# Performance work log

Hardware: AMD Instinct MI355X
Metric: run time of the kernel (lower is better)

## Reference

```python
import jax, jax.numpy as jnp
import numpy as np

B, SQ, SK, D, H, HD = 2, 2048, 2048, 1024, 16, 64


def setup_inputs() -> dict:
    key = jax.random.key(0)
    ks = jax.random.split(key, 10)
    s = 1.0 / np.sqrt(D)  # keep activations well-scaled
    return {
        "x": jax.random.normal(ks[0], (B, SQ, D), jnp.float32),
        "encoder_output": jax.random.normal(ks[1], (B, SK, D), jnp.float32),
        "Wq": jax.random.normal(ks[2], (H, D, HD), jnp.float32) * s,
        "bq": jax.random.normal(ks[3], (H, HD), jnp.float32) * 0.01,
        "Wk": jax.random.normal(ks[4], (H, D, HD), jnp.float32) * s,
        "bk": jax.random.normal(ks[5], (H, HD), jnp.float32) * 0.01,
        "Wv": jax.random.normal(ks[6], (H, D, HD), jnp.float32) * s,
        "bv": jax.random.normal(ks[7], (H, HD), jnp.float32) * 0.01,
        "Wo": jax.random.normal(ks[8], (D, D), jnp.float32) * s,
        "bo": jax.random.normal(ks[9], (D,), jnp.float32) * 0.01,
    }


def reference(x, encoder_output, Wq, bq, Wk, bk, Wv, bv, Wo, bo):
    # Batched per-head projections (equivalent to the per-head nn.Linear loop).
    q = jnp.einsum('bsd,hde->bhse', x, Wq) + bq[None, :, None, :]              # [B,H,SQ,HD]
    k = jnp.einsum('bsd,hde->bhse', encoder_output, Wk) + bk[None, :, None, :]  # [B,H,SK,HD]
    v = jnp.einsum('bsd,hde->bhse', encoder_output, Wv) + bv[None, :, None, :]  # [B,H,SK,HD]
    scale = 1.0 / jnp.sqrt(jnp.asarray(HD, q.dtype))
    scores = jnp.einsum('bhqe,bhke->bhqk', q, k) * scale                        # [B,H,SQ,SK]
    attn = jax.nn.softmax(scores, axis=-1)
    out = jnp.einsum('bhqk,bhke->bhqe', attn, v)                                # [B,H,SQ,HD]
    # concat heads along feature dim (head order matches torch.cat order)
    out = out.transpose(0, 2, 1, 3).reshape(out.shape[0], out.shape[2], -1)     # [B,SQ,D]
    # final linear; dropout is identity in eval mode
    return out @ Wo + bo
```

## Files before the change

### kernel.cpp

```cpp
#include <hip/hip_runtime.h>


typedef unsigned short u16;
typedef __bf16 bf16x8 __attribute__((ext_vector_type(8)));
typedef float f32x4 __attribute__((ext_vector_type(4)));
typedef float f32x16 __attribute__((ext_vector_type(16)));
typedef unsigned u32x2 __attribute__((ext_vector_type(2)));

#define B_ 2
#define SQ_ 2048
#define SK_ 2048
#define D_ 1024
#define H_ 16
#define HD_ 64

__device__ __forceinline__ u16 f2bf(float f) {
  union { float f; unsigned u; } c; c.f = f;
  unsigned u = c.u;
  return (u16)((u + 0x7fffu + ((u >> 16) & 1u)) >> 16);
}
__device__ __forceinline__ float bf2f(u16 h) {
  union { unsigned u; float f; } c; c.u = ((unsigned)h) << 16;
  return c.f;
}
__device__ __forceinline__ unsigned pack_bf16(float lo, float hi) {
  union { __bf16 h[2]; unsigned u; } c;
  c.h[0] = (__bf16)lo;
  c.h[1] = (__bf16)hi;
  return c.u;
}

#define GLOAD_LDS16(gp, lp)                                                  \
  __builtin_amdgcn_global_load_lds(                                          \
      (const __attribute__((address_space(1))) void*)(gp),                   \
      (__attribute__((address_space(3))) void*)(lp), 16, 0, 0)

__global__ __launch_bounds__(256) void prep_fused(const float* __restrict__ x,
                                                  const float* __restrict__ enc,
                                                  const float* __restrict__ Wq,
                                                  const float* __restrict__ Wk,
                                                  const float* __restrict__ Wv,
                                                  const float* __restrict__ Wo,
                                                  u16* __restrict__ xb,
                                                  u16* __restrict__ eb,
                                                  u16* __restrict__ WqT,
                                                  u16* __restrict__ WoT) {
  __shared__ float tile[64][65];
  const int id = blockIdx.x;
  const int tid = threadIdx.x;

  if (id < 8192) {
    const float* in = (id >= 4096) ? enc : x;
    u16* out = (id >= 4096) ? eb : xb;
    int i = (id & 4095) * 256 + tid;
    float4 v = ((const float4*)in)[i];
    uint2 p;
    p.x = (unsigned)f2bf(v.x) | ((unsigned)f2bf(v.y) << 16);
    p.y = (unsigned)f2bf(v.z) | ((unsigned)f2bf(v.w) << 16);
    ((uint2*)out)[i] = p;
    return;
  }

  if (id < 8960) {
    const int f = id - 8192;
    const int z48 = f >> 4, y = f & 15;
    const int mat = z48 >> 4, head = z48 & 15;
    const float* W = (mat == 0) ? Wq : (mat == 1 ? Wk : Wv);
    const float* ib = W + (long)head * 65536;
    u16* ob = WqT + ((long)mat << 20) + (long)head * 65536;
    const int r0 = y << 6;
#pragma unroll
    for (int i = 0; i < 16; ++i) {
      int idx = tid + (i << 8);
      int r = idx >> 6, c = idx & 63;
      tile[r][c] = ib[(long)(r0 + r) * 64 + c];
    }
    __syncthreads();
#pragma unroll
    for (int i = 0; i < 16; ++i) {
      int idx = tid + (i << 8);
      int cc = idx >> 6, rr = idx & 63;
      ob[(long)cc * 1024 + (r0 + rr)] = f2bf(tile[rr][cc]);
    }
    return;
  }

  {
    const int g = id - 8960;
    const int c0 = (g & 15) << 6, r0 = (g >> 4) << 6;
#pragma unroll
    for (int i = 0; i < 16; ++i) {
      int idx = tid + (i << 8);
      int r = idx >> 6, c = idx & 63;
      tile[r][c] = Wo[(long)(r0 + r) * 1024 + (c0 + c)];
    }
    __syncthreads();
#pragma unroll
    for (int i = 0; i < 16; ++i) {
      int idx = tid + (i << 8);
      int cc = idx >> 6, rr = idx & 63;
      WoT[(long)(c0 + cc) * 1024 + (r0 + rr)] = f2bf(tile[rr][cc]);
    }
  }
}

__global__ __launch_bounds__(256) void gemm_qkv(const u16* __restrict__ xb,
                                                const u16* __restrict__ eb,
                                                const u16* __restrict__ Wt3,
                                                const float* __restrict__ bq,
                                                const float* __restrict__ bk,
                                                const float* __restrict__ bv,
                                                u16* __restrict__ qws,
                                                u16* __restrict__ kws,
                                                u16* __restrict__ vT) {
  constexpr int M = 2048, N = 1024, K = 1024;
  __shared__ __align__(16) u16 As[128 * 64];
  __shared__ __align__(16) u16 Bs[128 * 64];
  const int tid = threadIdx.x;
  const int lane = tid & 63;
  const int wid = tid >> 6;
  const int l16 = lane & 15, quad = lane >> 4;
  const int wm = wid >> 1, wn = wid & 1;
  const int bn0g = blockIdx.x << 7;
  const int seg = bn0g >> 10;
  const int bn0 = bn0g & (N - 1);
  const int bm0 = blockIdx.y << 7;
  const u16* A = (seg == 0) ? xb : eb;
  const u16* Wt = Wt3 + ((long)seg << 20);
  const float* bias = (seg == 0) ? bq : (seg == 1 ? bk : bv);
  const long abase = (long)blockIdx.z * M * K;

  f32x4 acc[4][4];
#pragma unroll
  for (int i = 0; i < 4; ++i)
#pragma unroll
    for (int j = 0; j < 4; ++j) acc[i][j] = f32x4{0.f, 0.f, 0.f, 0.f};

  const int r0 = tid >> 3;
  const int c0s = ((tid & 7) ^ (r0 & 7)) << 3;
  const u16* agp = A + abase + (long)(bm0 + r0) * K + c0s;
  const u16* bgp = Wt + (long)(bn0 + r0) * K + c0s;
  u16* alp = As + tid * 8;
  u16* blp = Bs + tid * 8;

  for (int k0 = 0; k0 < K; k0 += 64) {
#pragma unroll
    for (int i = 0; i < 4; ++i) {
      GLOAD_LDS16(agp + k0 + (long)(32 * i) * K, alp + i * 2048);
      GLOAD_LDS16(bgp + k0 + (long)(32 * i) * K, blp + i * 2048);
    }
    __syncthreads();
#pragma unroll
    for (int kk = 0; kk < 2; ++kk) {
      const int csw = ((quad + 4 * kk) ^ (l16 & 7)) << 3;
      bf16x8 af[4], bfr[4];
#pragma unroll
      for (int mi = 0; mi < 4; ++mi)
        af[mi] = *(const bf16x8*)(As + (wm * 64 + mi * 16 + l16) * 64 + csw);
#pragma unroll
      for (int ni = 0; ni < 4; ++ni)
        bfr[ni] = *(const bf16x8*)(Bs + (wn * 64 + ni * 16 + l16) * 64 + csw);
#pragma unroll
      for (int mi = 0; mi < 4; ++mi)
#pragma unroll
        for (int ni = 0; ni < 4; ++ni)
          acc[mi][ni] = __builtin_amdgcn_mfma_f32_16x16x32_bf16(af[mi], bfr[ni],
                                                                acc[mi][ni], 0, 0, 0);
    }
    __syncthreads();
  }

  float bv4[4];
#pragma unroll
  for (int ni = 0; ni < 4; ++ni) bv4[ni] = bias[bn0 + wn * 64 + ni * 16 + l16];

  if (seg == 2) {
    const long zb = (long)blockIdx.z * N * M;
#pragma unroll
    for (int mi = 0; mi < 4; ++mi)
#pragma unroll
      for (int ni = 0; ni < 4; ++ni) {
        int colg = bn0 + wn * 64 + ni * 16 + l16;
        int rowg = bm0 + wm * 64 + mi * 16 + (quad << 2);
        ushort4 pk = make_ushort4(f2bf(acc[mi][ni][0] + bv4[ni]),
                                  f2bf(acc[mi][ni][1] + bv4[ni]),
                                  f2bf(acc[mi][ni][2] + bv4[ni]),
                                  f2bf(acc[mi][ni][3] + bv4[ni]));
        *(ushort4*)(vT + zb + (long)colg * M + rowg) = pk;
      }
  } else {
    u16* outp = seg ? kws : qws;
    const long cbase = (long)blockIdx.z * M * N;
#pragma unroll
    for (int mi = 0; mi < 4; ++mi)
#pragma unroll
      for (int ni = 0; ni < 4; ++ni)
#pragma unroll
        for (int r = 0; r < 4; ++r) {
          int row = bm0 + wm * 64 + mi * 16 + (quad << 2) + r;
          int col = bn0 + wn * 64 + ni * 16 + l16;
          outp[cbase + (long)row * N + col] = f2bf(acc[mi][ni][r] + bv4[ni]);
        }
  }
}

__global__ __launch_bounds__(256) void gemm_final(const u16* __restrict__ A,
                                                  const u16* __restrict__ Wt,
                                                  const float* __restrict__ bias,
                                                  float* __restrict__ C) {
  constexpr int M = 2048, N = 1024, K = 1024;
  __shared__ __align__(16) u16 As[64 * 64];
  __shared__ __align__(16) u16 Bs[128 * 64];
  const int tid = threadIdx.x;
  const int lane = tid & 63;
  const int wid = tid >> 6;
  const int l16 = lane & 15, quad = lane >> 4;
  const int bn0 = blockIdx.x << 7, bm0 = blockIdx.y << 6;

  f32x4 acc[4][2];
#pragma unroll
  for (int i = 0; i < 4; ++i)
#pragma unroll
    for (int j = 0; j < 2; ++j) acc[i][j] = f32x4{0.f, 0.f, 0.f, 0.f};

  const int r0 = tid >> 3;
  const int c0s = ((tid & 7) ^ (r0 & 7)) << 3;
  const long abase = (long)blockIdx.z * M * K;
  const u16* agp = A + abase + (long)(bm0 + r0) * K + c0s;
  const u16* bgp = Wt + (long)(bn0 + r0) * K + c0s;
  u16* alp = As + tid * 8;
  u16* blp = Bs + tid * 8;

  for (int k0 = 0; k0 < K; k0 += 64) {
#pragma unroll
    for (int i = 0; i < 2; ++i)
      GLOAD_LDS16(agp + k0 + (long)(32 * i) * K, alp + i * 2048);
#pragma unroll
    for (int i = 0; i < 4; ++i)
      GLOAD_LDS16(bgp + k0 + (long)(32 * i) * K, blp + i * 2048);
    __syncthreads();
#pragma unroll
    for (int kk = 0; kk < 2; ++kk) {
      const int csw = ((quad + 4 * kk) ^ (l16 & 7)) << 3;
      bf16x8 af[4], bfr[2];
#pragma unroll
      for (int mi = 0; mi < 4; ++mi)
        af[mi] = *(const bf16x8*)(As + (mi * 16 + l16) * 64 + csw);
#pragma unroll
      for (int ni = 0; ni < 2; ++ni)
        bfr[ni] = *(const bf16x8*)(Bs + (wid * 32 + ni * 16 + l16) * 64 + csw);
#pragma unroll
      for (int mi = 0; mi < 4; ++mi)
#pragma unroll
        for (int ni = 0; ni < 2; ++ni)
          acc[mi][ni] = __builtin_amdgcn_mfma_f32_16x16x32_bf16(af[mi], bfr[ni],
                                                                acc[mi][ni], 0, 0, 0);
    }
    __syncthreads();
  }

  float bv2[2];
#pragma unroll
  for (int ni = 0; ni < 2; ++ni) bv2[ni] = bias[bn0 + wid * 32 + ni * 16 + l16];
  const long cbase = (long)blockIdx.z * M * N;
#pragma unroll
  for (int mi = 0; mi < 4; ++mi)
#pragma unroll
    for (int ni = 0; ni < 2; ++ni)
#pragma unroll
      for (int r = 0; r < 4; ++r) {
        int row = bm0 + mi * 16 + (quad << 2) + r;
        int col = bn0 + wid * 32 + ni * 16 + l16;
        C[cbase + (long)row * N + col] = acc[mi][ni][r] + bv2[ni];
      }
}

#define ATTN_STAGE(kbase, vbase)                                              \
  do {                                                                        \
    GLOAD_LDS16(kp, (kbase) + tid * 8);                                       \
    GLOAD_LDS16(kp + (long)32 * D_, (kbase) + 2048 + tid * 8);                \
    GLOAD_LDS16(vp, (vbase) + tid * 8);                                       \
    GLOAD_LDS16(vp + (long)32 * SK_, (vbase) + 2048 + tid * 8);               \
    kp += (long)64 * D_;                                                      \
    vp += 64;                                                                 \
  } while (0)

#define QK_BLOCK(Kb, sx0, sx1)                                                \
  do {                                                                        \
    {                                                                         \
      bf16x8 kf0 = *(const bf16x8*)((Kb) + ro0 + sw[0]);                      \
      bf16x8 kf1 = *(const bf16x8*)((Kb) + 2048 + ro0 + sw[0]);               \
      sx0 = __builtin_amdgcn_mfma_f32_32x32x16_bf16(kf0, qf[0], ZV, 0, 0, 0); \
      sx1 = __builtin_amdgcn_mfma_f32_32x32x16_bf16(kf1, qf[0], ZV, 0, 0, 0); \
    }                                                                         \
    _Pragma("unroll") for (int j = 1; j < 4; ++j) {                           \
      bf16x8 kf0 = *(const bf16x8*)((Kb) + ro0 + sw[j]);                      \
      bf16x8 kf1 = *(const bf16x8*)((Kb) + 2048 + ro0 + sw[j]);               \
      sx0 = __builtin_amdgcn_mfma_f32_32x32x16_bf16(kf0, qf[j], sx0, 0, 0, 0);\
      sx1 = __builtin_amdgcn_mfma_f32_32x32x16_bf16(kf1, qf[j], sx1, 0, 0, 0);\
    }                                                                         \
  } while (0)

#define EXPD(sx0, sx1)                                                        \
  do {                                                                        \
    _Pragma("unroll") for (int g = 0; g < 8; ++g) {                           \
      float a0 = __expf(sx0[2 * g]);                                          \
      float a1 = __expf(sx0[2 * g + 1]);                                      \
      float b0 = __expf(sx1[2 * g]);                                          \
      float b1 = __expf(sx1[2 * g + 1]);                                      \
      psA += a0 + a1;                                                         \
      psB += b0 + b1;                                                         \
      d0[g] = pack_bf16(a0, a1);                                              \
      d1[g] = pack_bf16(b0, b1);                                              \
    }                                                                         \
  } while (0)

#define PV_KS(Vb, dd, k1, ks)                                                 \
  do {                                                                        \
    u32x2 sA = __builtin_amdgcn_permlane32_swap(dd[4 * (k1)],                 \
                                                dd[4 * (k1) + 2], false,      \
                                                false);                       \
    u32x2 sB = __builtin_amdgcn_permlane32_swap(dd[4 * (k1) + 1],             \
                                                dd[4 * (k1) + 3], false,      \
                                                false);                       \
    union { unsigned u[4]; bf16x8 v; } pa;                                    \
    pa.u[0] = sA[0]; pa.u[1] = sB[0]; pa.u[2] = sA[1]; pa.u[3] = sB[1];       \
    bf16x8 v0 = *(const bf16x8*)((Vb) + ro0 + sw[ks]);                        \
    bf16x8 v1 = *(const bf16x8*)((Vb) + 2048 + ro0 + sw[ks]);                 \
    o0 = __builtin_amdgcn_mfma_f32_32x32x16_bf16(pa.v, v0, o0, 0, 0, 0);      \
    o1 = __builtin_amdgcn_mfma_f32_32x32x16_bf16(pa.v, v1, o1, 0, 0, 0);      \
  } while (0)

#define PV4(Vb)                                                               \
  do {                                                                        \
    PV_KS(Vb, d0, 0, 0);                                                      \
    PV_KS(Vb, d0, 1, 1);                                                      \
    PV_KS(Vb, d1, 0, 2);                                                      \
    PV_KS(Vb, d1, 1, 3);                                                      \
  } while (0)

__global__ __launch_bounds__(256, 2) void attn_flash(const u16* __restrict__ q,
                                                     const u16* __restrict__ k,
                                                     const u16* __restrict__ vT,
                                                     u16* __restrict__ ctx) {
  __shared__ __align__(16) u16 Ks[2 * 4096];
  __shared__ __align__(16) u16 Vs[3 * 4096];

  const int tid = threadIdx.x;
  const int lane = tid & 63;
  const int wid = tid >> 6;
  const int l31 = lane & 31, h5 = lane >> 5;
  const int h = blockIdx.y, b = blockIdx.z;
  const int q0w = (blockIdx.x << 7) + (wid << 5);

  bf16x8 qf[4];
  const u16* qp = q + ((long)(b * SQ_ + q0w + l31) * D_ + h * HD_ + 8 * h5);
#pragma unroll
  for (int j = 0; j < 4; ++j) {
    bf16x8 t = *(const bf16x8*)(qp + 16 * j);
#pragma unroll
    for (int e = 0; e < 8; ++e) t[e] = (__bf16)((float)t[e] * 0.125f);
    qf[j] = t;
  }

  const int srow = tid >> 3;
  const int ssw = ((tid & 7) ^ (srow & 7)) << 3;
  const u16* kp = k + ((long)(b * SK_ + srow) * D_ + h * HD_ + ssw);
  const u16* vp = vT + ((long)(b * D_ + h * HD_ + srow) * SK_ + ssw);

  const int ro0 = l31 << 6;
  int sw[4];
#pragma unroll
  for (int i = 0; i < 4; ++i) sw[i] = ((2 * i + h5) ^ (lane & 7)) << 3;

  f32x16 o0, o1, sA0, sA1, sB0, sB1;
  f32x16 ZV = {};
#pragma unroll
  for (int i = 0; i < 16; ++i) { o0[i] = 0.f; o1[i] = 0.f; }
  float psA = 0.f, psB = 0.f;
  unsigned d0[8], d1[8];

  ATTN_STAGE(Ks, Vs);
  ATTN_STAGE(Ks + 4096, Vs + 4096);
  __syncthreads();
  QK_BLOCK(Ks, sA0, sA1);

  int viP = 0;
  int viS = 2;

  for (int tp = 0; tp < 30; tp += 2) {
    __syncthreads();
    ATTN_STAGE(Ks, Vs + viS * 4096);
    viS = (viS == 2) ? 0 : viS + 1;
    QK_BLOCK(Ks + 4096, sB0, sB1);
    EXPD(sA0, sA1);
    PV4(Vs + viP * 4096);
    viP = (viP == 2) ? 0 : viP + 1;

    __syncthreads();
    ATTN_STAGE(Ks + 4096, Vs + viS * 4096);
    viS = (viS == 2) ? 0 : viS + 1;
    QK_BLOCK(Ks, sA0, sA1);
    EXPD(sB0, sB1);
    PV4(Vs + viP * 4096);
    viP = (viP == 2) ? 0 : viP + 1;
  }
  __syncthreads();
  QK_BLOCK(Ks + 4096, sB0, sB1);
  EXPD(sA0, sA1);
  PV4(Vs + viP * 4096);
  viP = (viP == 2) ? 0 : viP + 1;
  __syncthreads();
  EXPD(sB0, sB1);
  PV4(Vs + viP * 4096);

  float ps = psA + psB;
  ps += __shfl_xor(ps, 32, 64);
  float inv = 1.f / ps;

#pragma unroll
  for (int r = 0; r < 16; ++r) {
    const int crow = (r & 3) + 8 * (r >> 2) + 4 * h5;
    float dq = __shfl(inv, crow, 64);
    long base = (long)(b * SQ_ + q0w + crow) * D_ + h * HD_ + l31;
    ctx[base] = f2bf(o0[r] * dq);
    ctx[base + 32] = f2bf(o1[r] * dq);
  }
}

extern "C" void kernel_launch(void* const* d_in, const int* in_sizes, int n_in,
                              void* d_out, int out_size, void* d_ws, size_t ws_size,
                              hipStream_t stream) {
  const float* x   = (const float*)d_in[0];
  const float* enc = (const float*)d_in[1];
  const float* Wq  = (const float*)d_in[2];
  const float* bq  = (const float*)d_in[3];
  const float* Wk  = (const float*)d_in[4];
  const float* bk  = (const float*)d_in[5];
  const float* Wv  = (const float*)d_in[6];
  const float* bv  = (const float*)d_in[7];
  const float* Wo  = (const float*)d_in[8];
  const float* bo  = (const float*)d_in[9];

  const long NE_X = (long)B_ * SQ_ * D_;
  const long NE_W = (long)D_ * D_;

  u16* outA = (u16*)d_out;
  u16* outB = outA + NE_X;
  u16* eb  = outB;
  u16* vTp = outA;

  u16* ws  = (u16*)d_ws;
  u16* WqT = ws;
  u16* WoT = WqT + 3 * NE_W;
  u16* qws = WoT + NE_W;
  u16* kws = qws + NE_X;
  u16* xb  = kws + NE_X;
  u16* ctx = xb;

  prep_fused<<<dim3(9216, 1, 1), 256, 0, stream>>>(x, enc, Wq, Wk, Wv, Wo,
                                                   xb, eb, WqT, WoT);

  gemm_qkv<<<dim3(24, 16, 2), 256, 0, stream>>>(xb, eb, WqT, bq, bk, bv,
                                                qws, kws, vTp);

  attn_flash<<<dim3(SQ_ / 128, H_, B_), 256, 0, stream>>>(qws, kws, vTp, ctx);

  gemm_final<<<dim3(8, 32, 2), 256, 0, stream>>>(ctx, WoT, bo, (float*)d_out);
}
```

Baseline: 207.1 us.

## Split attention keys across two warp groups per block and merge through LDS

The attention block grows to 512 threads. Each half of the block processes half of the key/value sequence into its own LDS staging buffers, so the serial loop is half as long. At the end, the upper half writes its partial output accumulators and row sums into LDS, and the lower half adds them, normalizes and writes ctx. This is meant to double the in-flight waves per query tile and shorten the per-block critical path. In exchange it adds an LDS reduction and uses more shared memory, and the stricter launch bounds (512,4) may force register spilling.

```diff
diff --git a/kernel.cpp b/kernel.cpp
--- a/kernel.cpp
+++ b/kernel.cpp
@@ -277,10 +277,10 @@
 
 #define ATTN_STAGE(kbase, vbase)                                              \
   do {                                                                        \
-    GLOAD_LDS16(kp, (kbase) + tid * 8);                                       \
-    GLOAD_LDS16(kp + (long)32 * D_, (kbase) + 2048 + tid * 8);                \
-    GLOAD_LDS16(vp, (vbase) + tid * 8);                                       \
-    GLOAD_LDS16(vp + (long)32 * SK_, (vbase) + 2048 + tid * 8);               \
+    GLOAD_LDS16(kp, (kbase) + st * 8);                                        \
+    GLOAD_LDS16(kp + (long)32 * D_, (kbase) + 2048 + st * 8);                 \
+    GLOAD_LDS16(vp, (vbase) + st * 8);                                        \
+    GLOAD_LDS16(vp + (long)32 * SK_, (vbase) + 2048 + st * 8);                \
     kp += (long)64 * D_;                                                      \
     vp += 64;                                                                 \
   } while (0)
@@ -339,19 +339,23 @@
     PV_KS(Vb, d1, 1, 3);                                                      \
   } while (0)
 
-__global__ __launch_bounds__(256, 2) void attn_flash(const u16* __restrict__ q,
+__global__ __launch_bounds__(512, 4) void attn_flash(const u16* __restrict__ q,
                                                      const u16* __restrict__ k,
                                                      const u16* __restrict__ vT,
                                                      u16* __restrict__ ctx) {
-  __shared__ __align__(16) u16 Ks[2 * 4096];
-  __shared__ __align__(16) u16 Vs[3 * 4096];
+  __shared__ __align__(16) u16 SM[40960];
 
   const int tid = threadIdx.x;
   const int lane = tid & 63;
   const int wid = tid >> 6;
+  const int half = wid >> 2;
+  const int wq = wid & 3;
   const int l31 = lane & 31, h5 = lane >> 5;
   const int h = blockIdx.y, b = blockIdx.z;
-  const int q0w = (blockIdx.x << 7) + (wid << 5);
+  const int q0w = (blockIdx.x << 7) + (wq << 5);
+
+  u16* Ksh = SM + half * 8192;
+  u16* Vsh = SM + 16384 + half * 12288;
 
   bf16x8 qf[4];
   const u16* qp = q + ((long)(b * SQ_ + q0w + l31) * D_ + h * HD_ + 8 * h5);
@@ -363,10 +367,11 @@
     qf[j] = t;
   }
 
-  const int srow = tid >> 3;
-  const int ssw = ((tid & 7) ^ (srow & 7)) << 3;
-  const u16* kp = k + ((long)(b * SK_ + srow) * D_ + h * HD_ + ssw);
-  const u16* vp = vT + ((long)(b * D_ + h * HD_ + srow) * SK_ + ssw);
+  const int st = tid & 255;
+  const int srow = st >> 3;
+  const int ssw = ((st & 7) ^ (srow & 7)) << 3;
+  const u16* kp = k + ((long)(b * SK_ + (half << 10) + srow) * D_ + h * HD_ + ssw);
+  const u16* vp = vT + ((long)(b * D_ + h * HD_ + srow) * SK_ + (half << 10) + ssw);
 
   const int ro0 = l31 << 6;
   int sw[4];
@@ -380,51 +385,70 @@
   float psA = 0.f, psB = 0.f;
   unsigned d0[8], d1[8];
 
-  ATTN_STAGE(Ks, Vs);
-  ATTN_STAGE(Ks + 4096, Vs + 4096);
+  ATTN_STAGE(Ksh, Vsh);
+  ATTN_STAGE(Ksh + 4096, Vsh + 4096);
   __syncthreads();
-  QK_BLOCK(Ks, sA0, sA1);
+  QK_BLOCK(Ksh, sA0, sA1);
 
   int viP = 0;
   int viS = 2;
 
-  for (int tp = 0; tp < 30; tp += 2) {
-    __syncthreads();
-    ATTN_STAGE(Ks, Vs + viS * 4096);
+  for (int tp = 0; tp < 14; tp += 2) {
+    __syncthreads();
+    ATTN_STAGE(Ksh, Vsh + viS * 4096);
     viS = (viS == 2) ? 0 : viS + 1;
-    QK_BLOCK(Ks + 4096, sB0, sB1);
+    QK_BLOCK(Ksh + 4096, sB0, sB1);
     EXPD(sA0, sA1);
-    PV4(Vs + viP * 4096);
+    PV4(Vsh + viP * 4096);
     viP = (viP == 2) ? 0 : viP + 1;
 
     __syncthreads();
-    ATTN_STAGE(Ks + 4096, Vs + viS * 4096);
+    ATTN_STAGE(Ksh + 4096, Vsh + viS * 4096);
     viS = (viS == 2) ? 0 : viS + 1;
-    QK_BLOCK(Ks, sA0, sA1);
+    QK_BLOCK(Ksh, sA0, sA1);
     EXPD(sB0, sB1);
-    PV4(Vs + viP * 4096);
+    PV4(Vsh + viP * 4096);
     viP = (viP == 2) ? 0 : viP + 1;
   }
   __syncthreads();
-  QK_BLOCK(Ks + 4096, sB0, sB1);
+  QK_BLOCK(Ksh + 4096, sB0, sB1);
   EXPD(sA0, sA1);
-  PV4(Vs + viP * 4096);
+  PV4(Vsh + viP * 4096);
   viP = (viP == 2) ? 0 : viP + 1;
-  __syncthreads();
   EXPD(sB0, sB1);
-  PV4(Vs + viP * 4096);
+  PV4(Vsh + viP * 4096);
 
   float ps = psA + psB;
   ps += __shfl_xor(ps, 32, 64);
-  float inv = 1.f / ps;
-
-#pragma unroll
-  for (int r = 0; r < 16; ++r) {
-    const int crow = (r & 3) + 8 * (r >> 2) + 4 * h5;
-    float dq = __shfl(inv, crow, 64);
-    long base = (long)(b * SQ_ + q0w + crow) * D_ + h * HD_ + l31;
-    ctx[base] = f2bf(o0[r] * dq);
-    ctx[base + 32] = f2bf(o1[r] * dq);
+
+  __syncthreads();
+  float* cb = (float*)SM;
+  const int wl = (wq << 6) | lane;
+  if (half) {
+#pragma unroll
+    for (int r = 0; r < 16; ++r) {
+      cb[r * 257 + wl] = o0[r];
+      cb[(r + 16) * 257 + wl] = o1[r];
+    }
+    cb[8300 + wl] = ps;
+  }
+  __syncthreads();
+  if (!half) {
+#pragma unroll
+    for (int r = 0; r < 16; ++r) {
+      o0[r] += cb[r * 257 + wl];
+      o1[r] += cb[(r + 16) * 257 + wl];
+    }
+    ps += cb[8300 + wl];
+    float inv = 1.f / ps;
+#pragma unroll
+    for (int r = 0; r < 16; ++r) {
+      const int crow = (r & 3) + 8 * (r >> 2) + 4 * h5;
+      float dq = __shfl(inv, crow, 64);
+      long base = (long)(b * SQ_ + q0w + crow) * D_ + h * HD_ + l31;
+      ctx[base] = f2bf(o0[r] * dq);
+      ctx[base + 32] = f2bf(o1[r] * dq);
+    }
   }
 }
 
@@ -464,7 +488,7 @@
   gemm_qkv<<<dim3(24, 16, 2), 256, 0, stream>>>(xb, eb, WqT, bq, bk, bv,
                                                 qws, kws, vTp);
 
-  attn_flash<<<dim3(SQ_ / 128, H_, B_), 256, 0, stream>>>(qws, kws, vTp, ctx);
+  attn_flash<<<dim3(SQ_ / 128, H_, B_), 512, 0, stream>>>(qws, kws, vTp, ctx);
 
   gemm_final<<<dim3(8, 32, 2), 256, 0, stream>>>(ctx, WoT, bo, (float*)d_out);
 }
```

New measurement: 318.2 us. 1.54x slower.
